# Optimization experiments

Hardware: AMD Instinct MI355X
Metric: run time of the kernel (lower is better)

The kernel has to match this reference:

```python
import jax, jax.numpy as jnp
import numpy as np

N = 50000
NEG_SLOPE = 0.2


def _glorot(key, shape):
    fan_in = shape[0]
    return jax.random.normal(key, shape, dtype=jnp.float32) / np.sqrt(fan_in)


def setup_inputs() -> dict:
    key = jax.random.key(0)
    ks = jax.random.split(key, 12)
    F_IN, H, C = 128, 128, 2
    E = 800000
    x = jax.random.normal(ks[0], (N, F_IN), dtype=jnp.float32)
    edge_index = jax.random.randint(ks[1], (2, E), 0, N, dtype=jnp.int64)
    return {
        "x": x,
        "edge_index": edge_index,
        # GATv2Conv 1: num_features -> hidden_units
        "Wl1": _glorot(ks[2], (F_IN, H)),
        "Wr1": _glorot(ks[3], (F_IN, H)),
        "att1": _glorot(ks[4], (H,)),
        "b1": jnp.zeros((H,), dtype=jnp.float32),
        # Linear skip 1
        "Wlin1": _glorot(ks[5], (F_IN, H)),
        "blin1": jnp.zeros((H,), dtype=jnp.float32),
        # GATv2Conv 2: hidden_units -> num_classes
        "Wl2": _glorot(ks[6], (H, C)),
        "Wr2": _glorot(ks[7], (H, C)),
        "att2": _glorot(ks[8], (C,)),
        "b2": jnp.zeros((C,), dtype=jnp.float32),
        # Linear skip 2
        "Wlin2": _glorot(ks[9], (H, C)),
        "blin2": jnp.zeros((C,), dtype=jnp.float32),
    }


def _gatv2_conv(x, src, dst, Wl, Wr, att, bias):
    # PyG GATv2Conv, heads=1: score = att . leaky_relu(Wl x_j + Wr x_i)
    xl = x @ Wl  # source-side transform [N, H]
    xr = x @ Wr  # target-side transform [N, H]
    m = xl[src] + xr[dst]  # [E, H]
    m = jnp.where(m > 0, m, NEG_SLOPE * m)
    e = m @ att  # [E]
    # segment softmax over incoming edges of each target node
    emax = jax.ops.segment_max(e, dst, num_segments=N)
    a = jnp.exp(e - emax[dst])
    denom = jax.ops.segment_sum(a, dst, num_segments=N)
    alpha = a / denom[dst]  # [E]
    out = jax.ops.segment_sum(alpha[:, None] * xl[src], dst, num_segments=N)
    return out + bias


def reference(x, edge_index, Wl1, Wr1, att1, b1, Wlin1, blin1,
              Wl2, Wr2, att2, b2, Wlin2, blin2):
    # add self loops (PyG default add_self_loops=True)
    loops = jnp.arange(N, dtype=edge_index.dtype)
    src = jnp.concatenate([edge_index[0], loops])
    dst = jnp.concatenate([edge_index[1], loops])

    h = _gatv2_conv(x, src, dst, Wl1, Wr1, att1, b1) + (x @ Wlin1 + blin1)
    h = jax.nn.relu(h)
    out = _gatv2_conv(h, src, dst, Wl2, Wr2, att2, b2) + (h @ Wlin2 + blin2)
    return (jax.nn.log_softmax(out, axis=1), edge_index)
```

## Files before the change

kernel.cpp:

```cpp
#include <hip/hip_runtime.h>
#include <math.h>

#define N_NODES 50000
#define F_IN 128
#define E_RAW 800000
#define E_TOT (E_RAW + N_NODES)
#define NEG_SLOPE 0.2f

#define TRR 128
#define TCC 64
#define KBB 32
#define XTS 132

__global__ __launch_bounds__(256, 4) void gemm1_kernel(
    const float* __restrict__ x,
    const float* __restrict__ Wl, const float* __restrict__ Wr,
    const float* __restrict__ Wlin,
    float* __restrict__ XL, float* __restrict__ XR, float* __restrict__ LIN)
{
    __shared__ float XT[KBB][XTS];
    __shared__ float WS[KBB][TCC];

    const int t  = threadIdx.x;
    const int tx = t & 15;
    const int ty = t >> 4;

    const int r0   = blockIdx.x * TRR;
    const int half = blockIdx.y & 1;
    const int mat  = blockIdx.y >> 1;
    const int cs0  = half * 64;

    const float* Wsel = (mat == 0) ? Wl : (mat == 1) ? Wr : Wlin;
    float*       Osel = (mat == 0) ? XL : (mat == 1) ? XR : LIN;

    const int sx_k4  = t & 7;
    const int sx_row = t >> 3;

    float acc[8][4];
    #pragma unroll
    for (int r = 0; r < 8; ++r)
        #pragma unroll
        for (int c = 0; c < 4; ++c) acc[r][c] = 0.f;

    for (int kc = 0; kc < 128; kc += KBB) {
        #pragma unroll
        for (int i = 0; i < 4; ++i) {
            const int row = sx_row + i * 32;
            const int gr  = r0 + row;
            float4 v = (gr < N_NODES)
                ? *(const float4*)(x + (size_t)gr * 128 + kc + sx_k4 * 4)
                : make_float4(0.f, 0.f, 0.f, 0.f);
            XT[sx_k4 * 4 + 0][row] = v.x;
            XT[sx_k4 * 4 + 1][row] = v.y;
            XT[sx_k4 * 4 + 2][row] = v.z;
            XT[sx_k4 * 4 + 3][row] = v.w;
        }
        #pragma unroll
        for (int i = 0; i < 2; ++i) {
            const int wk = (t >> 4) + i * 16;
            float4 wv = *(const float4*)(Wsel + (size_t)(kc + wk) * 128 + cs0 + tx * 4);
            *(float4*)&WS[wk][tx * 4] = wv;
        }
        __syncthreads();

        #pragma unroll 8
        for (int k = 0; k < KBB; ++k) {
            const float4 xlo = *(const float4*)&XT[k][ty * 8];
            const float4 xhi = *(const float4*)&XT[k][ty * 8 + 4];
            const float4 wv  = *(const float4*)&WS[k][tx * 4];
            const float xs[8] = {xlo.x, xlo.y, xlo.z, xlo.w,
                                 xhi.x, xhi.y, xhi.z, xhi.w};
            #pragma unroll
            for (int r = 0; r < 8; ++r) {
                acc[r][0] = fmaf(xs[r], wv.x, acc[r][0]);
                acc[r][1] = fmaf(xs[r], wv.y, acc[r][1]);
                acc[r][2] = fmaf(xs[r], wv.z, acc[r][2]);
                acc[r][3] = fmaf(xs[r], wv.w, acc[r][3]);
            }
        }
        __syncthreads();
    }

    #pragma unroll
    for (int r = 0; r < 8; ++r) {
        const int grow = r0 + ty * 8 + r;
        if (grow < N_NODES) {
            float4 o = make_float4(acc[r][0], acc[r][1], acc[r][2], acc[r][3]);
            *(float4*)(Osel + (size_t)grow * 128 + cs0 + tx * 4) = o;
        }
    }
}

__global__ __launch_bounds__(256) void hist_kernel(
    const int* __restrict__ eidx, int* __restrict__ counts)
{
    const int e = blockIdx.x * blockDim.x + threadIdx.x;
    if (e >= E_TOT) return;
    const int d = (e < E_RAW) ? eidx[E_RAW + e] : e - E_RAW;
    atomicAdd(&counts[d], 1);
}

__global__ __launch_bounds__(1024) void scan_kernel(
    const int* __restrict__ counts, int* __restrict__ rowptr, int* __restrict__ cursor)
{
    __shared__ int wsum[16];
    __shared__ int carry_s;
    const int tid = threadIdx.x, lane = tid & 63, wv = tid >> 6;
    if (tid == 0) carry_s = 0;
    __syncthreads();

    for (int base = 0; base < N_NODES; base += 1024) {
        const int i = base + tid;
        const int orig = (i < N_NODES) ? counts[i] : 0;
        int v = orig;
        #pragma unroll
        for (int off = 1; off < 64; off <<= 1) {
            int t = __shfl_up(v, off);
            if (lane >= off) v += t;
        }
        if (lane == 63) wsum[wv] = v;
        __syncthreads();
        if (wv == 0) {
            int s = (lane < 16) ? wsum[lane] : 0;
            #pragma unroll
            for (int off = 1; off < 16; off <<= 1) {
                int t = __shfl_up(s, off);
                if (lane >= off) s += t;
            }
            if (lane < 16) wsum[lane] = s;
        }
        __syncthreads();
        const int carry = carry_s;
        const int woff  = (wv == 0) ? 0 : wsum[wv - 1];
        const int excl  = carry + woff + v - orig;
        if (i < N_NODES) { rowptr[i] = excl; cursor[i] = excl; }
        __syncthreads();
        if (tid == 0) carry_s += wsum[15];
        __syncthreads();
    }
    if (threadIdx.x == 0) rowptr[N_NODES] = carry_s;
}

__global__ __launch_bounds__(256) void scatter_kernel(
    const int* __restrict__ eidx, int* __restrict__ cursor, int* __restrict__ csr_src)
{
    const int e = blockIdx.x * blockDim.x + threadIdx.x;
    if (e >= E_TOT) return;
    int s, d;
    if (e < E_RAW) { s = eidx[e]; d = eidx[E_RAW + e]; }
    else           { s = d = e - E_RAW; }
    const int pos = atomicAdd(&cursor[d], 1);
    csr_src[pos] = s;
}

__global__ __launch_bounds__(256) void fused1_kernel(
    const float* __restrict__ xl, const float* __restrict__ xr,
    const float* __restrict__ lin,
    const int* __restrict__ rowptr, const int* __restrict__ csr_src,
    const float* __restrict__ att, const float* __restrict__ b1,
    const float* __restrict__ blin1,
    float* __restrict__ h)
{
    const int gid  = blockIdx.x * blockDim.x + threadIdx.x;
    const int d    = gid >> 6;
    const int lane = gid & 63;
    if (d >= N_NODES) return;
    const int grp = lane >> 4;
    const int sub = lane & 15;

    const int r0 = rowptr[d], r1 = rowptr[d + 1];

    const float4 xr0 = *(const float4*)(xr + (size_t)d * 128 + sub * 8);
    const float4 xr1 = *(const float4*)(xr + (size_t)d * 128 + sub * 8 + 4);
    const float4 at0 = *(const float4*)(att + sub * 8);
    const float4 at1 = *(const float4*)(att + sub * 8 + 4);

    float num[8] = {0.f,0.f,0.f,0.f,0.f,0.f,0.f,0.f};
    float den = 0.f;

    for (int j = r0; j < r1; j += 4) {
        const int e  = j + grp;
        const int ee = (e < E_TOT) ? e : (E_TOT - 1);
        const int s  = csr_src[ee];
        const float4 a0 = *(const float4*)(xl + (size_t)s * 128 + sub * 8);
        const float4 a1 = *(const float4*)(xl + (size_t)s * 128 + sub * 8 + 4);

        float m, v = 0.f;
        m = a0.x + xr0.x; m = m > 0.f ? m : NEG_SLOPE * m; v = fmaf(m, at0.x, v);
        m = a0.y + xr0.y; m = m > 0.f ? m : NEG_SLOPE * m; v = fmaf(m, at0.y, v);
        m = a0.z + xr0.z; m = m > 0.f ? m : NEG_SLOPE * m; v = fmaf(m, at0.z, v);
        m = a0.w + xr0.w; m = m > 0.f ? m : NEG_SLOPE * m; v = fmaf(m, at0.w, v);
        m = a1.x + xr1.x; m = m > 0.f ? m : NEG_SLOPE * m; v = fmaf(m, at1.x, v);
        m = a1.y + xr1.y; m = m > 0.f ? m : NEG_SLOPE * m; v = fmaf(m, at1.y, v);
        m = a1.z + xr1.z; m = m > 0.f ? m : NEG_SLOPE * m; v = fmaf(m, at1.z, v);
        m = a1.w + xr1.w; m = m > 0.f ? m : NEG_SLOPE * m; v = fmaf(m, at1.w, v);

        v += __shfl_xor(v, 1);
        v += __shfl_xor(v, 2);
        v += __shfl_xor(v, 4);
        v += __shfl_xor(v, 8);

        const float ex = (e < r1) ? __expf(v) : 0.f;
        den += ex;
        num[0] = fmaf(ex, a0.x, num[0]);
        num[1] = fmaf(ex, a0.y, num[1]);
        num[2] = fmaf(ex, a0.z, num[2]);
        num[3] = fmaf(ex, a0.w, num[3]);
        num[4] = fmaf(ex, a1.x, num[4]);
        num[5] = fmaf(ex, a1.y, num[5]);
        num[6] = fmaf(ex, a1.z, num[6]);
        num[7] = fmaf(ex, a1.w, num[7]);
    }

    den += __shfl_xor(den, 16);
    den += __shfl_xor(den, 32);
    #pragma unroll
    for (int i = 0; i < 8; ++i) {
        num[i] += __shfl_xor(num[i], 16);
        num[i] += __shfl_xor(num[i], 32);
    }

    if (grp == 0) {
        const float inv = 1.f / den;
        const float4 l0  = *(const float4*)(lin   + (size_t)d * 128 + sub * 8);
        const float4 l1  = *(const float4*)(lin   + (size_t)d * 128 + sub * 8 + 4);
        const float4 bb0 = *(const float4*)(b1    + sub * 8);
        const float4 bb1 = *(const float4*)(b1    + sub * 8 + 4);
        const float4 bl0 = *(const float4*)(blin1 + sub * 8);
        const float4 bl1 = *(const float4*)(blin1 + sub * 8 + 4);
        float4 o0, o1;
        o0.x = fmaf(num[0], inv, bb0.x) + l0.x + bl0.x;
        o0.y = fmaf(num[1], inv, bb0.y) + l0.y + bl0.y;
        o0.z = fmaf(num[2], inv, bb0.z) + l0.z + bl0.z;
        o0.w = fmaf(num[3], inv, bb0.w) + l0.w + bl0.w;
        o1.x = fmaf(num[4], inv, bb1.x) + l1.x + bl1.x;
        o1.y = fmaf(num[5], inv, bb1.y) + l1.y + bl1.y;
        o1.z = fmaf(num[6], inv, bb1.z) + l1.z + bl1.z;
        o1.w = fmaf(num[7], inv, bb1.w) + l1.w + bl1.w;
        o0.x = o0.x > 0.f ? o0.x : 0.f;  o0.y = o0.y > 0.f ? o0.y : 0.f;
        o0.z = o0.z > 0.f ? o0.z : 0.f;  o0.w = o0.w > 0.f ? o0.w : 0.f;
        o1.x = o1.x > 0.f ? o1.x : 0.f;  o1.y = o1.y > 0.f ? o1.y : 0.f;
        o1.z = o1.z > 0.f ? o1.z : 0.f;  o1.w = o1.w > 0.f ? o1.w : 0.f;
        *(float4*)(h + (size_t)d * 128 + sub * 8)     = o0;
        *(float4*)(h + (size_t)d * 128 + sub * 8 + 4) = o1;
    }
}

__global__ __launch_bounds__(256) void gemm2_kernel(
    const float* __restrict__ h,
    const float* __restrict__ Wl2, const float* __restrict__ Wr2,
    const float* __restrict__ Wlin2,
    float* __restrict__ XL2, float* __restrict__ XR2, float* __restrict__ LIN2)
{
    const int gid  = blockIdx.x * blockDim.x + threadIdx.x;
    const int row  = gid >> 6;
    const int lane = gid & 63;
    if (row >= N_NODES) return;

    const float2 hv = ((const float2*)(h + (size_t)row * 128))[lane];
    const int k0 = 2 * lane, k1 = 2 * lane + 1;

    float v[6];
    v[0] = hv.x * Wl2[k0*2+0]   + hv.y * Wl2[k1*2+0];
    v[1] = hv.x * Wl2[k0*2+1]   + hv.y * Wl2[k1*2+1];
    v[2] = hv.x * Wr2[k0*2+0]   + hv.y * Wr2[k1*2+0];
    v[3] = hv.x * Wr2[k0*2+1]   + hv.y * Wr2[k1*2+1];
    v[4] = hv.x * Wlin2[k0*2+0] + hv.y * Wlin2[k1*2+0];
    v[5] = hv.x * Wlin2[k0*2+1] + hv.y * Wlin2[k1*2+1];

    #pragma unroll
    for (int off = 32; off > 0; off >>= 1) {
        #pragma unroll
        for (int j = 0; j < 6; ++j) v[j] += __shfl_xor(v[j], off);
    }

    if (lane == 0) {
        XL2[row*2+0]  = v[0]; XL2[row*2+1]  = v[1];
        XR2[row*2+0]  = v[2]; XR2[row*2+1]  = v[3];
        LIN2[row*2+0] = v[4]; LIN2[row*2+1] = v[5];
    }
}

__global__ __launch_bounds__(256) void fused2_kernel(
    const float* __restrict__ XL2, const float* __restrict__ XR2,
    const float* __restrict__ LIN2,
    const int* __restrict__ rowptr, const int* __restrict__ csr_src,
    const float* __restrict__ att2, const float* __restrict__ b2,
    const float* __restrict__ blin2,
    float* __restrict__ out)
{
    const int d = blockIdx.x * blockDim.x + threadIdx.x;
    if (d >= N_NODES) return;

    const int r0 = rowptr[d], r1 = rowptr[d + 1];
    const float xr0 = XR2[d*2+0], xr1 = XR2[d*2+1];
    const float a0 = att2[0], a1 = att2[1];

    float num0 = 0.f, num1 = 0.f, den = 0.f;
    for (int j = r0; j < r1; ++j) {
        const int s = csr_src[j];
        const float l0 = XL2[s*2+0], l1 = XL2[s*2+1];
        float m0 = l0 + xr0, m1 = l1 + xr1;
        m0 = m0 > 0.f ? m0 : NEG_SLOPE * m0;
        m1 = m1 > 0.f ? m1 : NEG_SLOPE * m1;
        const float ex = __expf(m0 * a0 + m1 * a1);
        den += ex;
        num0 = fmaf(ex, l0, num0);
        num1 = fmaf(ex, l1, num1);
    }
    const float inv = 1.f / den;
    const float o0 = num0 * inv + b2[0] + LIN2[d*2+0] + blin2[0];
    const float o1 = num1 * inv + b2[1] + LIN2[d*2+1] + blin2[1];
    const float mx  = fmaxf(o0, o1);
    const float lse = mx + logf(__expf(o0 - mx) + __expf(o1 - mx));
    out[d*2+0] = o0 - lse;
    out[d*2+1] = o1 - lse;
}

__global__ __launch_bounds__(256) void copy_eidx_kernel(
    const int* __restrict__ eidx, float* __restrict__ out)
{
    const int i = blockIdx.x * blockDim.x + threadIdx.x;
    if (i >= 2 * E_RAW) return;
    out[i] = (float)eidx[i];
}

extern "C" void kernel_launch(void* const* d_in, const int* in_sizes, int n_in,
                              void* d_out, int out_size, void* d_ws, size_t ws_size,
                              hipStream_t stream)
{
    const float* x      = (const float*)d_in[0];
    const int*   eidx   = (const int*)  d_in[1];
    const float* Wl1    = (const float*)d_in[2];
    const float* Wr1    = (const float*)d_in[3];
    const float* att1   = (const float*)d_in[4];
    const float* b1     = (const float*)d_in[5];
    const float* Wlin1  = (const float*)d_in[6];
    const float* blin1  = (const float*)d_in[7];
    const float* Wl2    = (const float*)d_in[8];
    const float* Wr2    = (const float*)d_in[9];
    const float* att2   = (const float*)d_in[10];
    const float* b2     = (const float*)d_in[11];
    const float* Wlin2  = (const float*)d_in[12];
    const float* blin2  = (const float*)d_in[13];

    float* out = (float*)d_out;

    float* ws     = (float*)d_ws;
    float* XL     = ws;
    float* XR     = ws + 6400000;
    float* LIN    = ws + 12800000;
    int*   counts = (int*)(ws + 19200000);
    int*   rowptr = counts + 50000;
    int*   csr    = rowptr + 50001;
    float* H      = XR;
    float* XL2    = LIN;
    float* XR2    = LIN + 100000;
    float* LIN2   = LIN + 200000;

    {
        dim3 grid((N_NODES + TRR - 1) / TRR, 6);
        gemm1_kernel<<<grid, 256, 0, stream>>>(x, Wl1, Wr1, Wlin1, XL, XR, LIN);
    }

    hipMemsetAsync(counts, 0, N_NODES * sizeof(int), stream);
    hist_kernel<<<(E_TOT + 255) / 256, 256, 0, stream>>>(eidx, counts);
    scan_kernel<<<1, 1024, 0, stream>>>(counts, rowptr, counts);
    scatter_kernel<<<(E_TOT + 255) / 256, 256, 0, stream>>>(eidx, counts, csr);

    {
        const int blocks = (N_NODES * 64 + 255) / 256;
        fused1_kernel<<<blocks, 256, 0, stream>>>(XL, XR, LIN, rowptr, csr,
                                                  att1, b1, blin1, H);
    }

    {
        const int blocks = (N_NODES * 64 + 255) / 256;
        gemm2_kernel<<<blocks, 256, 0, stream>>>(H, Wl2, Wr2, Wlin2, XL2, XR2, LIN2);
    }
    {
        const int blocks = (N_NODES + 255) / 256;
        fused2_kernel<<<blocks, 256, 0, stream>>>(XL2, XR2, LIN2, rowptr, csr,
                                                  att2, b2, blin2, out);
    }
    {
        const int blocks = (2 * E_RAW + 255) / 256;
        copy_eidx_kernel<<<blocks, 256, 0, stream>>>(eidx, out + (size_t)N_NODES * 2);
    }
}
```

Before: 407.7 us.

## Fuse layer-2 projections into aggregation, parallelize layer-2 softmax, re-layout GEMM tile

The second-layer projections (Wl2, Wr2, Wlin2) are folded into the first aggregation kernel. It now computes ReLU(h) in registers and reduces the 2-wide dot products across 16 lanes, so the 50000x128 hidden tensor is never written or re-read and one launch goes away. The second aggregation now uses 16 lanes per node with a shuffle reduction instead of one serial thread per node. The small layer-2 intermediates are placed in a part of the output buffer that the edge-index copy overwrites later. The first GEMM also stores its x tile row-major with 33-float padding instead of transposed: the shared-memory stores become conflict-free, but the inner loop now issues scalar LDS reads instead of float4 reads.

```diff
diff --git a/kernel.cpp b/kernel.cpp
--- a/kernel.cpp
+++ b/kernel.cpp
@@ -10,7 +10,7 @@
 #define TRR 128
 #define TCC 64
 #define KBB 32
-#define XTS 132
+#define XP33 33
 
 __global__ __launch_bounds__(256, 4) void gemm1_kernel(
     const float* __restrict__ x,
@@ -18,7 +18,7 @@
     const float* __restrict__ Wlin,
     float* __restrict__ XL, float* __restrict__ XR, float* __restrict__ LIN)
 {
-    __shared__ float XT[KBB][XTS];
+    __shared__ float XS[TRR][XP33];
     __shared__ float WS[KBB][TCC];
 
     const int t  = threadIdx.x;
@@ -50,10 +50,10 @@
             float4 v = (gr < N_NODES)
                 ? *(const float4*)(x + (size_t)gr * 128 + kc + sx_k4 * 4)
                 : make_float4(0.f, 0.f, 0.f, 0.f);
-            XT[sx_k4 * 4 + 0][row] = v.x;
-            XT[sx_k4 * 4 + 1][row] = v.y;
-            XT[sx_k4 * 4 + 2][row] = v.z;
-            XT[sx_k4 * 4 + 3][row] = v.w;
+            XS[row][sx_k4 * 4 + 0] = v.x;
+            XS[row][sx_k4 * 4 + 1] = v.y;
+            XS[row][sx_k4 * 4 + 2] = v.z;
+            XS[row][sx_k4 * 4 + 3] = v.w;
         }
         #pragma unroll
         for (int i = 0; i < 2; ++i) {
@@ -65,17 +65,16 @@
 
         #pragma unroll 8
         for (int k = 0; k < KBB; ++k) {
-            const float4 xlo = *(const float4*)&XT[k][ty * 8];
-            const float4 xhi = *(const float4*)&XT[k][ty * 8 + 4];
-            const float4 wv  = *(const float4*)&WS[k][tx * 4];
-            const float xs[8] = {xlo.x, xlo.y, xlo.z, xlo.w,
-                                 xhi.x, xhi.y, xhi.z, xhi.w};
+            const float4 wv = *(const float4*)&WS[k][tx * 4];
+            float xv[8];
+            #pragma unroll
+            for (int r = 0; r < 8; ++r) xv[r] = XS[ty * 8 + r][k];
             #pragma unroll
             for (int r = 0; r < 8; ++r) {
-                acc[r][0] = fmaf(xs[r], wv.x, acc[r][0]);
-                acc[r][1] = fmaf(xs[r], wv.y, acc[r][1]);
-                acc[r][2] = fmaf(xs[r], wv.z, acc[r][2]);
-                acc[r][3] = fmaf(xs[r], wv.w, acc[r][3]);
+                acc[r][0] = fmaf(xv[r], wv.x, acc[r][0]);
+                acc[r][1] = fmaf(xv[r], wv.y, acc[r][1]);
+                acc[r][2] = fmaf(xv[r], wv.z, acc[r][2]);
+                acc[r][3] = fmaf(xv[r], wv.w, acc[r][3]);
             }
         }
         __syncthreads();
@@ -159,7 +158,9 @@
     const int* __restrict__ rowptr, const int* __restrict__ csr_src,
     const float* __restrict__ att, const float* __restrict__ b1,
     const float* __restrict__ blin1,
-    float* __restrict__ h)
+    const float* __restrict__ Wl2, const float* __restrict__ Wr2,
+    const float* __restrict__ Wlin2,
+    float* __restrict__ XL2, float* __restrict__ XR2, float* __restrict__ LIN2)
 {
     const int gid  = blockIdx.x * blockDim.x + threadIdx.x;
     const int d    = gid >> 6;
@@ -220,64 +221,61 @@
         num[i] += __shfl_xor(num[i], 32);
     }
 
-    if (grp == 0) {
-        const float inv = 1.f / den;
-        const float4 l0  = *(const float4*)(lin   + (size_t)d * 128 + sub * 8);
-        const float4 l1  = *(const float4*)(lin   + (size_t)d * 128 + sub * 8 + 4);
-        const float4 bb0 = *(const float4*)(b1    + sub * 8);
-        const float4 bb1 = *(const float4*)(b1    + sub * 8 + 4);
-        const float4 bl0 = *(const float4*)(blin1 + sub * 8);
-        const float4 bl1 = *(const float4*)(blin1 + sub * 8 + 4);
-        float4 o0, o1;
-        o0.x = fmaf(num[0], inv, bb0.x) + l0.x + bl0.x;
-        o0.y = fmaf(num[1], inv, bb0.y) + l0.y + bl0.y;
-        o0.z = fmaf(num[2], inv, bb0.z) + l0.z + bl0.z;
-        o0.w = fmaf(num[3], inv, bb0.w) + l0.w + bl0.w;
-        o1.x = fmaf(num[4], inv, bb1.x) + l1.x + bl1.x;
-        o1.y = fmaf(num[5], inv, bb1.y) + l1.y + bl1.y;
-        o1.z = fmaf(num[6], inv, bb1.z) + l1.z + bl1.z;
-        o1.w = fmaf(num[7], inv, bb1.w) + l1.w + bl1.w;
-        o0.x = o0.x > 0.f ? o0.x : 0.f;  o0.y = o0.y > 0.f ? o0.y : 0.f;
-        o0.z = o0.z > 0.f ? o0.z : 0.f;  o0.w = o0.w > 0.f ? o0.w : 0.f;
-        o1.x = o1.x > 0.f ? o1.x : 0.f;  o1.y = o1.y > 0.f ? o1.y : 0.f;
-        o1.z = o1.z > 0.f ? o1.z : 0.f;  o1.w = o1.w > 0.f ? o1.w : 0.f;
-        *(float4*)(h + (size_t)d * 128 + sub * 8)     = o0;
-        *(float4*)(h + (size_t)d * 128 + sub * 8 + 4) = o1;
-    }
-}
-
-__global__ __launch_bounds__(256) void gemm2_kernel(
-    const float* __restrict__ h,
-    const float* __restrict__ Wl2, const float* __restrict__ Wr2,
-    const float* __restrict__ Wlin2,
-    float* __restrict__ XL2, float* __restrict__ XR2, float* __restrict__ LIN2)
-{
-    const int gid  = blockIdx.x * blockDim.x + threadIdx.x;
-    const int row  = gid >> 6;
-    const int lane = gid & 63;
-    if (row >= N_NODES) return;
-
-    const float2 hv = ((const float2*)(h + (size_t)row * 128))[lane];
-    const int k0 = 2 * lane, k1 = 2 * lane + 1;
-
-    float v[6];
-    v[0] = hv.x * Wl2[k0*2+0]   + hv.y * Wl2[k1*2+0];
-    v[1] = hv.x * Wl2[k0*2+1]   + hv.y * Wl2[k1*2+1];
-    v[2] = hv.x * Wr2[k0*2+0]   + hv.y * Wr2[k1*2+0];
-    v[3] = hv.x * Wr2[k0*2+1]   + hv.y * Wr2[k1*2+1];
-    v[4] = hv.x * Wlin2[k0*2+0] + hv.y * Wlin2[k1*2+0];
-    v[5] = hv.x * Wlin2[k0*2+1] + hv.y * Wlin2[k1*2+1];
-
-    #pragma unroll
-    for (int off = 32; off > 0; off >>= 1) {
-        #pragma unroll
-        for (int j = 0; j < 6; ++j) v[j] += __shfl_xor(v[j], off);
-    }
-
+    const float inv = 1.f / den;
+    const float4 l0  = *(const float4*)(lin   + (size_t)d * 128 + sub * 8);
+    const float4 l1  = *(const float4*)(lin   + (size_t)d * 128 + sub * 8 + 4);
+    const float4 bb0 = *(const float4*)(b1    + sub * 8);
+    const float4 bb1 = *(const float4*)(b1    + sub * 8 + 4);
+    const float4 bl0 = *(const float4*)(blin1 + sub * 8);
+    const float4 bl1 = *(const float4*)(blin1 + sub * 8 + 4);
+    float h0 = fmaf(num[0], inv, bb0.x) + l0.x + bl0.x;
+    float h1 = fmaf(num[1], inv, bb0.y) + l0.y + bl0.y;
+    float h2 = fmaf(num[2], inv, bb0.z) + l0.z + bl0.z;
+    float h3 = fmaf(num[3], inv, bb0.w) + l0.w + bl0.w;
+    float h4 = fmaf(num[4], inv, bb1.x) + l1.x + bl1.x;
+    float h5 = fmaf(num[5], inv, bb1.y) + l1.y + bl1.y;
+    float h6 = fmaf(num[6], inv, bb1.z) + l1.z + bl1.z;
+    float h7 = fmaf(num[7], inv, bb1.w) + l1.w + bl1.w;
+    h0 = h0 > 0.f ? h0 : 0.f;  h1 = h1 > 0.f ? h1 : 0.f;
+    h2 = h2 > 0.f ? h2 : 0.f;  h3 = h3 > 0.f ? h3 : 0.f;
+    h4 = h4 > 0.f ? h4 : 0.f;  h5 = h5 > 0.f ? h5 : 0.f;
+    h6 = h6 > 0.f ? h6 : 0.f;  h7 = h7 > 0.f ? h7 : 0.f;
+
+    float pl0, pl1, pr0, pr1, pn0, pn1;
+    {
+        const float4 a = ((const float4*)Wl2)[sub*4+0];
+        const float4 b = ((const float4*)Wl2)[sub*4+1];
+        const float4 c = ((const float4*)Wl2)[sub*4+2];
+        const float4 e4= ((const float4*)Wl2)[sub*4+3];
+        pl0 = h0*a.x + h1*a.z + h2*b.x + h3*b.z + h4*c.x + h5*c.z + h6*e4.x + h7*e4.z;
+        pl1 = h0*a.y + h1*a.w + h2*b.y + h3*b.w + h4*c.y + h5*c.w + h6*e4.y + h7*e4.w;
+    }
+    {
+        const float4 a = ((const float4*)Wr2)[sub*4+0];
+        const float4 b = ((const float4*)Wr2)[sub*4+1];
+        const float4 c = ((const float4*)Wr2)[sub*4+2];
+        const float4 e4= ((const float4*)Wr2)[sub*4+3];
+        pr0 = h0*a.x + h1*a.z + h2*b.x + h3*b.z + h4*c.x + h5*c.z + h6*e4.x + h7*e4.z;
+        pr1 = h0*a.y + h1*a.w + h2*b.y + h3*b.w + h4*c.y + h5*c.w + h6*e4.y + h7*e4.w;
+    }
+    {
+        const float4 a = ((const float4*)Wlin2)[sub*4+0];
+        const float4 b = ((const float4*)Wlin2)[sub*4+1];
+        const float4 c = ((const float4*)Wlin2)[sub*4+2];
+        const float4 e4= ((const float4*)Wlin2)[sub*4+3];
+        pn0 = h0*a.x + h1*a.z + h2*b.x + h3*b.z + h4*c.x + h5*c.z + h6*e4.x + h7*e4.z;
+        pn1 = h0*a.y + h1*a.w + h2*b.y + h3*b.w + h4*c.y + h5*c.w + h6*e4.y + h7*e4.w;
+    }
+    #pragma unroll
+    for (int off = 1; off < 16; off <<= 1) {
+        pl0 += __shfl_xor(pl0, off); pl1 += __shfl_xor(pl1, off);
+        pr0 += __shfl_xor(pr0, off); pr1 += __shfl_xor(pr1, off);
+        pn0 += __shfl_xor(pn0, off); pn1 += __shfl_xor(pn1, off);
+    }
     if (lane == 0) {
-        XL2[row*2+0]  = v[0]; XL2[row*2+1]  = v[1];
-        XR2[row*2+0]  = v[2]; XR2[row*2+1]  = v[3];
-        LIN2[row*2+0] = v[4]; LIN2[row*2+1] = v[5];
+        XL2[d*2+0]  = pl0; XL2[d*2+1]  = pl1;
+        XR2[d*2+0]  = pr0; XR2[d*2+1]  = pr1;
+        LIN2[d*2+0] = pn0; LIN2[d*2+1] = pn1;
     }
 }
 
@@ -289,32 +287,42 @@
     const float* __restrict__ blin2,
     float* __restrict__ out)
 {
-    const int d = blockIdx.x * blockDim.x + threadIdx.x;
+    const int gid = blockIdx.x * blockDim.x + threadIdx.x;
+    const int d   = gid >> 4;
+    const int l16 = gid & 15;
     if (d >= N_NODES) return;
 
     const int r0 = rowptr[d], r1 = rowptr[d + 1];
-    const float xr0 = XR2[d*2+0], xr1 = XR2[d*2+1];
+    const float2 xrv = *(const float2*)(XR2 + (size_t)d * 2);
     const float a0 = att2[0], a1 = att2[1];
 
     float num0 = 0.f, num1 = 0.f, den = 0.f;
-    for (int j = r0; j < r1; ++j) {
+    for (int j = r0 + l16; j < r1; j += 16) {
         const int s = csr_src[j];
-        const float l0 = XL2[s*2+0], l1 = XL2[s*2+1];
-        float m0 = l0 + xr0, m1 = l1 + xr1;
+        const float2 l = *(const float2*)(XL2 + (size_t)s * 2);
+        float m0 = l.x + xrv.x, m1 = l.y + xrv.y;
         m0 = m0 > 0.f ? m0 : NEG_SLOPE * m0;
         m1 = m1 > 0.f ? m1 : NEG_SLOPE * m1;
-        const float ex = __expf(m0 * a0 + m1 * a1);
+        const float ex = __expf(fmaf(m0, a0, m1 * a1));
         den += ex;
-        num0 = fmaf(ex, l0, num0);
-        num1 = fmaf(ex, l1, num1);
-    }
-    const float inv = 1.f / den;
-    const float o0 = num0 * inv + b2[0] + LIN2[d*2+0] + blin2[0];
-    const float o1 = num1 * inv + b2[1] + LIN2[d*2+1] + blin2[1];
-    const float mx  = fmaxf(o0, o1);
-    const float lse = mx + logf(__expf(o0 - mx) + __expf(o1 - mx));
-    out[d*2+0] = o0 - lse;
-    out[d*2+1] = o1 - lse;
+        num0 = fmaf(ex, l.x, num0);
+        num1 = fmaf(ex, l.y, num1);
+    }
+    #pragma unroll
+    for (int off = 1; off < 16; off <<= 1) {
+        den  += __shfl_xor(den,  off);
+        num0 += __shfl_xor(num0, off);
+        num1 += __shfl_xor(num1, off);
+    }
+    if (l16 == 0) {
+        const float inv = 1.f / den;
+        const float o0 = num0 * inv + b2[0] + LIN2[d*2+0] + blin2[0];
+        const float o1 = num1 * inv + b2[1] + LIN2[d*2+1] + blin2[1];
+        const float mx  = fmaxf(o0, o1);
+        const float lse = mx + logf(__expf(o0 - mx) + __expf(o1 - mx));
+        out[d*2+0] = o0 - lse;
+        out[d*2+1] = o1 - lse;
+    }
 }
 
 __global__ __launch_bounds__(256) void copy_eidx_kernel(
@@ -353,10 +361,9 @@
     int*   counts = (int*)(ws + 19200000);
     int*   rowptr = counts + 50000;
     int*   csr    = rowptr + 50001;
-    float* H      = XR;
-    float* XL2    = LIN;
-    float* XR2    = LIN + 100000;
-    float* LIN2   = LIN + 200000;
+    float* XL2    = out + 100000;
+    float* XR2    = out + 200000;
+    float* LIN2   = out + 300000;
 
     {
         dim3 grid((N_NODES + TRR - 1) / TRR, 6);
@@ -371,18 +378,17 @@
     {
         const int blocks = (N_NODES * 64 + 255) / 256;
         fused1_kernel<<<blocks, 256, 0, stream>>>(XL, XR, LIN, rowptr, csr,
-                                                  att1, b1, blin1, H);
-    }
-
-    {
-        const int blocks = (N_NODES * 64 + 255) / 256;
-        gemm2_kernel<<<blocks, 256, 0, stream>>>(H, Wl2, Wr2, Wlin2, XL2, XR2, LIN2);
-    }
-    {
-        const int blocks = (N_NODES + 255) / 256;
+                                                  att1, b1, blin1,
+                                                  Wl2, Wr2, Wlin2,
+                                                  XL2, XR2, LIN2);
+    }
+
+    {
+        const int blocks = (N_NODES * 16 + 255) / 256;
         fused2_kernel<<<blocks, 256, 0, stream>>>(XL2, XR2, LIN2, rowptr, csr,
                                                   att2, b2, blin2, out);
     }
+
     {
         const int blocks = (2 * E_RAW + 255) / 256;
         copy_eidx_kernel<<<blocks, 256, 0, stream>>>(eidx, out + (size_t)N_NODES * 2);
```

Result: faster. 392.5 us (-3.7%).
